# Optimization experiments

Hardware: AMD Instinct MI355X
Metric: run time of the kernel (lower is better)

The kernel has to match this reference:

```python
import jax, jax.numpy as jnp
import numpy as np

# config matching init_kwargs: stox_params=[4,2,1,1,64,2], in=64, out=128, k=3, pad=1
A_BITS = 4          # a_slices = a_bits / a_bits_per_stream = 4
W_SLICES = 2        # w_bits / w_bits_per_slice = 2
NUM_CHUNKS = 9      # ceil(64*9/64)
SUB = 64            # crossbar chunk width
ITERS = 2           # stochastic iterations
EPS = 1e-5          # BatchNorm1d eps


def ste(y, x):
    # straight-through estimator: forward y, backward identity of x
    return x + jax.lax.stop_gradient(y - x)


def unfold3x3(x):
    # torch F.unfold(x, 3, dilation=1, padding=1, stride=1): [B,C,H,W] -> [B, C*9, H*W]
    B, C, H, W = x.shape
    xp = jnp.pad(x, ((0, 0), (0, 0), (1, 1), (1, 1)))
    cols = [xp[:, :, i:i + H, j:j + W] for i in range(3) for j in range(3)]
    return jnp.stack(cols, axis=2).reshape(B, C * 9, H * W)  # (c, kh, kw) ordering


def setup_inputs() -> dict:
    key = jax.random.key(0)
    k1, k2 = jax.random.split(key)
    inputs = jax.random.normal(k1, (8, 64, 32, 32), jnp.float32)
    fan_in = 64 * 9  # kaiming_normal_ fan_in
    weight = jax.random.normal(k2, (128 * W_SLICES, 64, 3, 3), jnp.float32) * np.float32(np.sqrt(2.0 / fan_in))
    bn_gamma = jnp.ones((128 * W_SLICES,), jnp.float32)
    bn_beta = jnp.zeros((128 * W_SLICES,), jnp.float32)
    return {"inputs": inputs, "weight": weight, "bn_gamma": bn_gamma, "bn_beta": bn_beta}


def reference(inputs, weight, bn_gamma, bn_beta):
    O = weight.shape[0]  # out_channels * W_SLICES = 256
    # --- per-output-row weight standardization + 1-bit STE quantization (WeightQuantize) ---
    wf = weight.reshape(O, -1)                       # [O, Cin*9]
    bw = wf - wf.mean(-1, keepdims=True)
    bw = bw / bw.std(-1, ddof=1, keepdims=True)      # torch std is unbiased
    qw = ste(jnp.sign(bw), bw)                       # [O, Cin*9]
    # --- unfold + multi-bit input stream (create_input_stream): bit-planes stacked on batch dim ---
    a = unfold3x3(inputs)                            # [B, Cin*9, L]
    Bsz, C9, L = a.shape
    x = jnp.clip(a, 0.0, 1.0)
    q = jnp.round(x * (2 ** A_BITS - 1))
    bits = jnp.stack([jnp.floor(q / (2 ** i)) % 2 for i in range(A_BITS)], 0)  # [A,B,C9,L]
    qa = bits.reshape(A_BITS * Bsz, C9, L)
    # --- chunked crossbar linear + BatchNorm1d(train) + MTJ sign, summed over chunks/iterations ---
    out = jnp.zeros((A_BITS * Bsz, O, L), a.dtype)
    for c in range(NUM_CHUNKS):
        wk = qa[:, c * SUB:(c + 1) * SUB, :]         # [B', SUB, L]
        ww = qw[:, c * SUB:(c + 1) * SUB]            # [O, SUB]
        for _ in range(ITERS):
            lin = jnp.einsum('bcl,oc->bol', wk, ww)  # [B', O, L]
            mu = lin.mean((0, 2), keepdims=True)
            var = lin.var((0, 2), keepdims=True)     # biased, as torch BN training
            bn = bn_gamma[None, :, None] * (lin - mu) / jnp.sqrt(var + EPS) + bn_beta[None, :, None]
            out = out + ste(jnp.sign(bn), bn)        # MTJ stochastic comparator -> sign w/ STE
    # --- bit-weighted reconstructions ---
    wvec = (2.0 ** jnp.arange(W_SLICES, dtype=a.dtype)) / (2 ** W_SLICES - 1)
    out = jnp.einsum('s,bsol->bol', wvec, out.reshape(A_BITS * Bsz, W_SLICES, O // W_SLICES, L))
    avec = (2.0 ** jnp.arange(A_BITS, dtype=a.dtype)) / (2 ** A_BITS - 1)
    out = jnp.einsum('a,abol->bol', avec, out.reshape(A_BITS, Bsz, O // W_SLICES, L))
    # --- F.fold with (1,1) kernel == reshape to square spatial map ---
    P = int(np.sqrt(L))
    return out.reshape(Bsz, O // W_SLICES, P, P)
```

## Files before the change

### kernel.cpp

```cpp
#include <hip/hip_runtime.h>
#include <cstdint>
#include <cstddef>

static const size_t OFF_ACT  = 0;
static const size_t OFF_W    = OFF_ACT + 2359296;
static const size_t OFF_T    = OFF_W   + 18432;
static const size_t OFF_NS1  = OFF_T   + 18432;
static const size_t OFF_MUG  = OFF_NS1 + 9216;
static const size_t OFF_FLAG = OFF_MUG + 18432;
static const size_t OFF_WB   = OFF_FLAG + 1024;
static const size_t OFF_CQ   = OFF_WB + 147456;
static const size_t OFF_FF   = OFF_CQ + 9216;

typedef int v4i __attribute__((ext_vector_type(4)));

__device__ __forceinline__ int isgn(int e) {
  int t = e < -1 ? -1 : e;
  return t > 1 ? 1 : t;
}

__global__ __launch_bounds__(256) void k_prep(const float* __restrict__ x,
                                              const float* __restrict__ w,
                                              const float* __restrict__ gamma,
                                              const float* __restrict__ beta,
                                              int* __restrict__ T,
                                              uint64_t* __restrict__ act,
                                              uint64_t* __restrict__ wbits,
                                              int* __restrict__ flag,
                                              signed char* __restrict__ wbyte,
                                              int* __restrict__ flagF) {
  int bid = blockIdx.x;
  int tid = threadIdx.x;
  if (bid < 512) {
    int base = bid << 10;
    int vals[9];
#pragma unroll
    for (int k = 0; k < 9; ++k) vals[k] = 0;
#pragma unroll
    for (int i = 0; i < 4; ++i) {
      int px = tid + i * 256;
      int h = px >> 5, ww = px & 31;
      float v = x[base + px];
      v = fminf(fmaxf(v, 0.f), 1.f);
      int q = (int)rintf(v * 15.f);
      int pc = __popc((unsigned)q);
      vals[0] += pc;
      if (h == 0) vals[1] += pc;
      if (h == 31) vals[2] += pc;
      if (ww == 0) vals[3] += pc;
      if (ww == 31) vals[4] += pc;
      if (h == 0 && ww == 0) vals[5] += pc;
      if (h == 0 && ww == 31) vals[6] += pc;
      if (h == 31 && ww == 0) vals[7] += pc;
      if (h == 31 && ww == 31) vals[8] += pc;
    }
#pragma unroll
    for (int k = 0; k < 9; ++k)
      for (int off = 32; off; off >>= 1) vals[k] += __shfl_down(vals[k], off, 64);
    __shared__ int red[4][9];
    int wid = tid >> 6, lane = tid & 63;
    if (lane == 0)
#pragma unroll
      for (int k = 0; k < 9; ++k) red[wid][k] = vals[k];
    __syncthreads();
    if (tid < 9) T[bid * 9 + tid] = red[0][tid] + red[1][tid] + red[2][tid] + red[3][tid];
  } else if (bid < 1664) {
    int blk = bid - 512;
    int bc = blk >> 4;
    int c = bc % 9, b = bc / 9;
    int l0 = (blk & 15) << 6;
    int h0 = l0 >> 5;
    int chLo = (c * 64) / 9;
    __shared__ unsigned char qlds[8][4][34];
    for (int e = tid; e < 1024; e += 256) {
      int ci = e >> 7, rem = e & 127, ri = rem >> 5, wi = rem & 31;
      int hh = h0 - 1 + ri;
      int qv = 0;
      if ((unsigned)hh < 32u) {
        float v = x[((b * 64 + chLo + ci) << 10) + (hh << 5) + wi];
        v = fminf(fmaxf(v, 0.f), 1.f);
        qv = (int)rintf(v * 15.f);
      }
      qlds[ci][ri][wi + 1] = (unsigned char)qv;
      if (wi == 0) qlds[ci][ri][0] = 0;
      if (wi == 31) qlds[ci][ri][33] = 0;
    }
    __syncthreads();

    int half = tid & 3;
    int dl = tid >> 2;
    int l = l0 + dl;
    int h = l >> 5, w0 = l & 31;
    int hr = h - h0;
    int i9 = c * 64 + half * 16;
    int ch = i9 / 9;
    int k = i9 - ch * 9;
    int ki = k / 3, kj = k - ki * 3;
    int cch = ch - chLo;
    unsigned m0 = 0, m1 = 0, m2 = 0, m3 = 0;
#pragma unroll
    for (int jj = 0; jj < 16; ++jj) {
      int q = qlds[cch][hr + ki][w0 + kj];
      m0 |= (unsigned)(q & 1) << jj;
      m1 |= (unsigned)((q >> 1) & 1) << jj;
      m2 |= (unsigned)((q >> 2) & 1) << jj;
      m3 |= (unsigned)((q >> 3) & 1) << jj;
      if (++kj == 3) { kj = 0; if (++ki == 3) { ki = 0; ++cch; } }
    }
    size_t stride = 8 * 9 * 1024;
    size_t off = ((size_t)b * 9 + c) * 1024 + l;
    unsigned short* a16 = (unsigned short*)act;
    a16[(0 * stride + off) * 4 + half] = (unsigned short)m0;
    a16[(1 * stride + off) * 4 + half] = (unsigned short)m1;
    a16[(2 * stride + off) * 4 + half] = (unsigned short)m2;
    a16[(3 * stride + off) * 4 + half] = (unsigned short)m3;
  } else {
    int lane = tid & 63;
    int wid = tid >> 6;
    int o = (bid - 1664) * 4 + wid;
    const float* row = w + (size_t)o * 576;
    double s = 0.0;
#pragma unroll
    for (int i = 0; i < 9; ++i) s += (double)row[lane + i * 64];
    for (int off = 32; off; off >>= 1) s += __shfl_down(s, off, 64);
    s = __shfl(s, 0, 64);
    float mean = (float)(s / 576.0);
#pragma unroll
    for (int c = 0; c < 9; ++c) {
      float v = row[c * 64 + lane];
      int pos = (v - mean) > 0.f;
      unsigned long long m = __ballot(pos);
      if (lane == 0) wbits[o * 9 + c] = (uint64_t)m;
      wbyte[(c * 256 + o) * 64 + lane] = pos ? (signed char)1 : (signed char)-1;
    }
    if (lane == 0) {
      int f = (beta[o] == 0.f && gamma[o] > 0.f) ? 1 : 0;
      flag[o] = f;
      flagF[o] = f;
    }
  }
}

__global__ __launch_bounds__(256) void k_s1(const int* __restrict__ T,
                                            const uint64_t* __restrict__ wbits,
                                            const int* __restrict__ flag,
                                            const float* __restrict__ gamma,
                                            const uint64_t* __restrict__ act,
                                            int* __restrict__ negS1,
                                            int* __restrict__ cq,
                                            int* __restrict__ flagF,
                                            float2* __restrict__ MUG) {
  __shared__ int Tsh[576];
  __shared__ int Ush[9 * 65];
  int tid = threadIdx.x;
  for (int i = tid; i < 576; i += 256) {
    int acc = 0;
#pragma unroll
    for (int b = 0; b < 8; ++b) acc += T[b * 576 + i];
    Tsh[i] = acc;
  }
  __syncthreads();
  for (int i = tid; i < 576; i += 256) {
    int ch = i / 9;
    int k = i - ch * 9;
    int ki = k / 3, kj = k - ki * 3;
    const int* t = &Tsh[ch * 9];
    int u = t[0];
    if (ki == 0) u -= t[2]; else if (ki == 2) u -= t[1];
    if (kj == 0) u -= t[4]; else if (kj == 2) u -= t[3];
    if (ki == 0 && kj == 0) u += t[8];
    if (ki == 0 && kj == 2) u += t[7];
    if (ki == 2 && kj == 0) u += t[6];
    if (ki == 2 && kj == 2) u += t[5];
    Ush[(i >> 6) * 65 + (i & 63)] = u;
  }
  __syncthreads();
  int pair = blockIdx.x * 256 + tid;
  int o = pair / 9, c = pair - o * 9;
  uint64_t wv = wbits[pair];
  int tot = 0, pos = 0;
#pragma unroll 8
  for (int j = 0; j < 64; ++j) {
    int cnt = Ush[c * 65 + j];
    tot += cnt;
    if ((wv >> j) & 1) pos += cnt;
  }
  int s1 = 2 * pos - tot;
  negS1[c * 256 + o] = -s1;
  cq[c * 256 + o] = -(s1 >> 15);
  if ((s1 & 32767) == 0) atomicAnd(&flagF[o], 0);
  if (!flag[o]) {
    int s2 = 0;
    for (int i = 0; i < 32768; ++i) {
      uint64_t av = act[((size_t)(i >> 10) * 9 + c) * 1024 + (i & 1023)];
      int lin = 2 * __popcll(av & wv) - __popcll(av);
      s2 += lin * lin;
    }
    float mu = (float)s1 * (1.f / 32768.f);
    float ex2 = (float)s2 * (1.f / 32768.f);
    float var = ex2 - mu * mu;
    if (var < 0.f) var = 0.f;
    MUG[pair] = make_float2(mu, gamma[o] / sqrtf(var + 1e-5f));
  }
}

__global__ __launch_bounds__(256, 2) void k_out(const uint64_t* __restrict__ act,
                                                const signed char* __restrict__ wbyte,
                                                const int* __restrict__ negS1g,
                                                const int* __restrict__ cqg,
                                                const float2* __restrict__ MUG,
                                                const int* __restrict__ flag,
                                                const int* __restrict__ flagF,
                                                const float* __restrict__ beta,
                                                float* __restrict__ out) {
  __shared__ __align__(16) int cqsh[2304];
  int tid = threadIdx.x;
  int lt = blockIdx.x;
  int b = blockIdx.y;
  for (int i = tid; i < 2304; i += 256) cqsh[i] = cqg[i];
  __syncthreads();

  int lane = tid & 63;
  int w = __builtin_amdgcn_readfirstlane(tid >> 6);
  int row = lane & 15;
  int g = lane >> 4;
  int sh16 = (g & 1) * 16;

  int o0 = w * 32 + (lane & 31);
  int fb = flagF[o0] & flagF[o0 + 128];
  bool fastAll = (bool)__all(fb != 0);

  const v4i zacc = {0, 0, 0, 0};
  int l = lt * 16 + row;
  const char* actbyte = (const char*)act + ((size_t)b * 9 * 1024 + l) * 8 + (g >> 1) * 4;

  if (fastAll) {
    int P[4][4];
#pragma unroll
    for (int q = 0; q < 4; ++q)
#pragma unroll
      for (int r = 0; r < 4; ++r) P[q][r] = 0;

    for (int c = 0; c < 9; ++c) {
      v4i Af[4], Cin[4];
#pragma unroll
      for (int q = 0; q < 4; ++q) {
        int ot = 2 * w + (q & 1) + (q >> 1) * 8;
        Af[q] = *(const v4i*)(wbyte + ((size_t)(c * 256 + ot * 16 + row) * 64 + g * 16));
        Cin[q] = *(const v4i*)&cqsh[c * 256 + ot * 16 + g * 4];
      }
      unsigned dwv[4];
#pragma unroll
      for (int a = 0; a < 4; ++a)
        dwv[a] = *(const unsigned*)(actbyte + (size_t)a * 589824 + (size_t)c * 8192);

      int pc[4][4];
#pragma unroll
      for (int q = 0; q < 4; ++q)
#pragma unroll
        for (int r = 0; r < 4; ++r) pc[q][r] = 0;

#pragma unroll
      for (int ai = 0; ai < 4; ++ai) {
        int a = 3 - ai;
        unsigned bits = (dwv[a] >> sh16) & 0xFFFFu;
        v4i Bf;
#pragma unroll
        for (int d = 0; d < 4; ++d)
          Bf[d] = (int)((((bits >> (4 * d)) & 0xFu) * 0x00204081u) & 0x01010101u);
#pragma unroll
        for (int q = 0; q < 4; ++q) {
          v4i acc = __builtin_amdgcn_mfma_i32_16x16x64_i8(Af[q], Bf, Cin[q], 0, 0, 0);
#pragma unroll
          for (int r = 0; r < 4; ++r)
            pc[q][r] += pc[q][r] + (acc[r] > 0 ? 1 : 0);
        }
      }
#pragma unroll
      for (int q = 0; q < 4; ++q)
#pragma unroll
        for (int r = 0; r < 4; ++r) P[q][r] += pc[q][r];
    }
#pragma unroll
    for (int q2 = 0; q2 < 2; ++q2)
#pragma unroll
      for (int r = 0; r < 4; ++r) {
        int oo = (2 * w + q2) * 16 + g * 4 + r;
        int M = 2 * (P[q2][r] + 2 * P[q2 + 2][r]) - 405;
        out[((size_t)b * 128 + oo) * 1024 + l] = (float)M * (2.f / 45.f);
      }
  } else {
    int M[2][4] = {{0, 0, 0, 0}, {0, 0, 0, 0}};
    float F[2][4] = {{0.f, 0.f, 0.f, 0.f}, {0.f, 0.f, 0.f, 0.f}};
    int flv[4][4];
#pragma unroll
    for (int q = 0; q < 4; ++q) {
      int ot = 2 * w + (q & 1) + (q >> 1) * 8;
#pragma unroll
      for (int r = 0; r < 4; ++r) flv[q][r] = flag[ot * 16 + g * 4 + r];
    }
    for (int c = 0; c < 9; ++c) {
      v4i Af[4];
      int nS[4][4];
#pragma unroll
      for (int q = 0; q < 4; ++q) {
        int ot = 2 * w + (q & 1) + (q >> 1) * 8;
        Af[q] = *(const v4i*)(wbyte + ((size_t)(c * 256 + ot * 16 + row) * 64 + g * 16));
#pragma unroll
        for (int r = 0; r < 4; ++r) nS[q][r] = negS1g[c * 256 + ot * 16 + g * 4 + r];
      }
      unsigned dwv[4];
#pragma unroll
      for (int a = 0; a < 4; ++a)
        dwv[a] = *(const unsigned*)(actbyte + (size_t)a * 589824 + (size_t)c * 8192);
#pragma unroll
      for (int a = 0; a < 4; ++a) {
        unsigned bits = (dwv[a] >> sh16) & 0xFFFFu;
        v4i Bf;
#pragma unroll
        for (int d = 0; d < 4; ++d)
          Bf[d] = (int)((((bits >> (4 * d)) & 0xFu) * 0x00204081u) & 0x01010101u);
#pragma unroll
        for (int q = 0; q < 4; ++q) {
          v4i acc = __builtin_amdgcn_mfma_i32_16x16x64_i8(Af[q], Bf, zacc, 0, 0, 0);
          int ot = 2 * w + (q & 1) + (q >> 1) * 8;
#pragma unroll
          for (int r = 0; r < 4; ++r) {
            int lin = acc[r];
            if (flv[q][r]) {
              M[q & 1][r] += isgn((lin << 15) + nS[q][r]) << (a + (q >> 1));
            } else {
              int o = ot * 16 + g * 4 + r;
              float2 m2 = MUG[o * 9 + c];
              float bn = m2.y * ((float)lin - m2.x) + beta[o];
              float sg = (bn > 0.f) ? 1.f : ((bn < 0.f) ? -1.f : 0.f);
              F[q & 1][r] += sg * (float)(1 << (a + (q >> 1)));
            }
          }
        }
      }
    }
#pragma unroll
    for (int q2 = 0; q2 < 2; ++q2)
#pragma unroll
      for (int r = 0; r < 4; ++r) {
        int oo = (2 * w + q2) * 16 + g * 4 + r;
        out[((size_t)b * 128 + oo) * 1024 + l] =
            ((float)M[q2][r] + F[q2][r]) * (2.f / 45.f);
      }
  }
}

extern "C" void kernel_launch(void* const* d_in, const int* in_sizes, int n_in,
                              void* d_out, int out_size, void* d_ws, size_t ws_size,
                              hipStream_t stream) {
  const float* inputs = (const float*)d_in[0];
  const float* weight = (const float*)d_in[1];
  const float* gamma = (const float*)d_in[2];
  const float* beta = (const float*)d_in[3];
  float* out = (float*)d_out;

  char* ws = (char*)d_ws;
  uint64_t* act = (uint64_t*)(ws + OFF_ACT);
  uint64_t* wbits = (uint64_t*)(ws + OFF_W);
  int* T = (int*)(ws + OFF_T);
  int* negS1 = (int*)(ws + OFF_NS1);
  float2* MUG = (float2*)(ws + OFF_MUG);
  int* flag = (int*)(ws + OFF_FLAG);
  signed char* wbyte = (signed char*)(ws + OFF_WB);
  int* cq = (int*)(ws + OFF_CQ);
  int* flagF = (int*)(ws + OFF_FF);

  k_prep<<<1728, 256, 0, stream>>>(inputs, weight, gamma, beta, T, act, wbits, flag, wbyte, flagF);
  k_s1<<<9, 256, 0, stream>>>(T, wbits, flag, gamma, act, negS1, cq, flagF, MUG);
  k_out<<<dim3(64, 8), 256, 0, stream>>>(act, wbyte, negS1, cq, MUG, flag, flagF, beta, out);
}
```

Baseline: 89.15 us.

## Split activation bit-planes across two wave groups with LDS reduction in k_out

Doubles the k_out block to 512 threads. The upper four waves handle activation bit-planes 2-3 and the lower four handle planes 0-1, so each wave runs half the MFMA chain per chunk. Partial counts from the upper waves go through shared memory and are combined with a factor of four before the final store. This adds parallelism per output tile, since the grid is only 512 blocks, at the cost of an extra LDS buffer, a barrier and duplicated weight loads.

```diff
diff --git a/kernel.cpp b/kernel.cpp
--- a/kernel.cpp
+++ b/kernel.cpp
@@ -204,7 +204,7 @@
   }
 }
 
-__global__ __launch_bounds__(256, 2) void k_out(const uint64_t* __restrict__ act,
+__global__ __launch_bounds__(512, 4) void k_out(const uint64_t* __restrict__ act,
                                                 const signed char* __restrict__ wbyte,
                                                 const int* __restrict__ negS1g,
                                                 const int* __restrict__ cqg,
@@ -214,17 +214,21 @@
                                                 const float* __restrict__ beta,
                                                 float* __restrict__ out) {
   __shared__ __align__(16) int cqsh[2304];
+  __shared__ unsigned int part[4][16][65];
   int tid = threadIdx.x;
   int lt = blockIdx.x;
   int b = blockIdx.y;
-  for (int i = tid; i < 2304; i += 256) cqsh[i] = cqg[i];
+  for (int i = tid; i < 2304; i += 512) cqsh[i] = cqg[i];
   __syncthreads();
 
   int lane = tid & 63;
-  int w = __builtin_amdgcn_readfirstlane(tid >> 6);
+  int w8 = __builtin_amdgcn_readfirstlane(tid >> 6);
+  int w = w8 & 3;
+  int hi = w8 >> 2;
   int row = lane & 15;
   int g = lane >> 4;
   int sh16 = (g & 1) * 16;
+  int aBase = 2 * hi;
 
   int o0 = w * 32 + (lane & 31);
   int fb = flagF[o0] & flagF[o0 + 128];
@@ -233,6 +237,8 @@
   const v4i zacc = {0, 0, 0, 0};
   int l = lt * 16 + row;
   const char* actbyte = (const char*)act + ((size_t)b * 9 * 1024 + l) * 8 + (g >> 1) * 4;
+
+  unsigned pt[16];
 
   if (fastAll) {
     int P[4][4];
@@ -249,10 +255,12 @@
         Af[q] = *(const v4i*)(wbyte + ((size_t)(c * 256 + ot * 16 + row) * 64 + g * 16));
         Cin[q] = *(const v4i*)&cqsh[c * 256 + ot * 16 + g * 4];
       }
-      unsigned dwv[4];
-#pragma unroll
-      for (int a = 0; a < 4; ++a)
-        dwv[a] = *(const unsigned*)(actbyte + (size_t)a * 589824 + (size_t)c * 8192);
+      unsigned dwv[2];
+#pragma unroll
+      for (int ai = 0; ai < 2; ++ai)
+        dwv[ai] = *(const unsigned*)(actbyte +
+                                     (size_t)(aBase + ai) * 589824 +
+                                     (size_t)c * 8192);
 
       int pc[4][4];
 #pragma unroll
@@ -261,9 +269,9 @@
         for (int r = 0; r < 4; ++r) pc[q][r] = 0;
 
 #pragma unroll
-      for (int ai = 0; ai < 4; ++ai) {
-        int a = 3 - ai;
-        unsigned bits = (dwv[a] >> sh16) & 0xFFFFu;
+      for (int ai2 = 0; ai2 < 2; ++ai2) {
+        int ai = 1 - ai2;
+        unsigned bits = (dwv[ai] >> sh16) & 0xFFFFu;
         v4i Bf;
 #pragma unroll
         for (int d = 0; d < 4; ++d)
@@ -282,16 +290,12 @@
         for (int r = 0; r < 4; ++r) P[q][r] += pc[q][r];
     }
 #pragma unroll
-    for (int q2 = 0; q2 < 2; ++q2)
-#pragma unroll
-      for (int r = 0; r < 4; ++r) {
-        int oo = (2 * w + q2) * 16 + g * 4 + r;
-        int M = 2 * (P[q2][r] + 2 * P[q2 + 2][r]) - 405;
-        out[((size_t)b * 128 + oo) * 1024 + l] = (float)M * (2.f / 45.f);
-      }
+    for (int q = 0; q < 4; ++q)
+#pragma unroll
+      for (int r = 0; r < 4; ++r) pt[q * 4 + r] = (unsigned)P[q][r];
   } else {
-    int M[2][4] = {{0, 0, 0, 0}, {0, 0, 0, 0}};
-    float F[2][4] = {{0.f, 0.f, 0.f, 0.f}, {0.f, 0.f, 0.f, 0.f}};
+    int M2[2][4] = {{0, 0, 0, 0}, {0, 0, 0, 0}};
+    float F2[2][4] = {{0.f, 0.f, 0.f, 0.f}, {0.f, 0.f, 0.f, 0.f}};
     int flv[4][4];
 #pragma unroll
     for (int q = 0; q < 4; ++q) {
@@ -309,13 +313,15 @@
 #pragma unroll
         for (int r = 0; r < 4; ++r) nS[q][r] = negS1g[c * 256 + ot * 16 + g * 4 + r];
       }
-      unsigned dwv[4];
-#pragma unroll
-      for (int a = 0; a < 4; ++a)
-        dwv[a] = *(const unsigned*)(actbyte + (size_t)a * 589824 + (size_t)c * 8192);
-#pragma unroll
-      for (int a = 0; a < 4; ++a) {
-        unsigned bits = (dwv[a] >> sh16) & 0xFFFFu;
+      unsigned dwv[2];
+#pragma unroll
+      for (int ai = 0; ai < 2; ++ai)
+        dwv[ai] = *(const unsigned*)(actbyte +
+                                     (size_t)(aBase + ai) * 589824 +
+                                     (size_t)c * 8192);
+#pragma unroll
+      for (int ai = 0; ai < 2; ++ai) {
+        unsigned bits = (dwv[ai] >> sh16) & 0xFFFFu;
         v4i Bf;
 #pragma unroll
         for (int d = 0; d < 4; ++d)
@@ -328,13 +334,13 @@
           for (int r = 0; r < 4; ++r) {
             int lin = acc[r];
             if (flv[q][r]) {
-              M[q & 1][r] += isgn((lin << 15) + nS[q][r]) << (a + (q >> 1));
+              M2[q & 1][r] += isgn((lin << 15) + nS[q][r]) << (ai + (q >> 1));
             } else {
               int o = ot * 16 + g * 4 + r;
               float2 m2 = MUG[o * 9 + c];
               float bn = m2.y * ((float)lin - m2.x) + beta[o];
               float sg = (bn > 0.f) ? 1.f : ((bn < 0.f) ? -1.f : 0.f);
-              F[q & 1][r] += sg * (float)(1 << (a + (q >> 1)));
+              F2[q & 1][r] += sg * (float)(1 << (ai + (q >> 1)));
             }
           }
         }
@@ -344,10 +350,45 @@
     for (int q2 = 0; q2 < 2; ++q2)
 #pragma unroll
       for (int r = 0; r < 4; ++r) {
-        int oo = (2 * w + q2) * 16 + g * 4 + r;
-        out[((size_t)b * 128 + oo) * 1024 + l] =
-            ((float)M[q2][r] + F[q2][r]) * (2.f / 45.f);
-      }
+        pt[q2 * 4 + r] = (unsigned)M2[q2][r];
+        pt[8 + q2 * 4 + r] = __float_as_uint(F2[q2][r]);
+      }
+  }
+
+  if (hi) {
+#pragma unroll
+    for (int i = 0; i < 16; ++i) part[w][i][lane] = pt[i];
+  }
+  __syncthreads();
+  if (!hi) {
+    if (fastAll) {
+      int Pf[4][4];
+#pragma unroll
+      for (int q = 0; q < 4; ++q)
+#pragma unroll
+        for (int r = 0; r < 4; ++r)
+          Pf[q][r] = (int)pt[q * 4 + r] + 4 * (int)part[w][q * 4 + r][lane];
+#pragma unroll
+      for (int q2 = 0; q2 < 2; ++q2)
+#pragma unroll
+        for (int r = 0; r < 4; ++r) {
+          int oo = (2 * w + q2) * 16 + g * 4 + r;
+          int M = 2 * (Pf[q2][r] + 2 * Pf[q2 + 2][r]) - 405;
+          out[((size_t)b * 128 + oo) * 1024 + l] = (float)M * (2.f / 45.f);
+        }
+    } else {
+#pragma unroll
+      for (int q2 = 0; q2 < 2; ++q2)
+#pragma unroll
+        for (int r = 0; r < 4; ++r) {
+          int oo = (2 * w + q2) * 16 + g * 4 + r;
+          int Mf = (int)pt[q2 * 4 + r] + 4 * (int)part[w][q2 * 4 + r][lane];
+          float Ff = __uint_as_float(pt[8 + q2 * 4 + r]) +
+                     4.f * __uint_as_float(part[w][8 + q2 * 4 + r][lane]);
+          out[((size_t)b * 128 + oo) * 1024 + l] =
+              ((float)Mf + Ff) * (2.f / 45.f);
+        }
+    }
   }
 }
 
@@ -373,5 +414,5 @@
 
   k_prep<<<1728, 256, 0, stream>>>(inputs, weight, gamma, beta, T, act, wbits, flag, wbyte, flagF);
   k_s1<<<9, 256, 0, stream>>>(T, wbits, flag, gamma, act, negS1, cq, flagF, MUG);
-  k_out<<<dim3(64, 8), 256, 0, stream>>>(act, wbyte, negS1, cq, MUG, flag, flagF, beta, out);
+  k_out<<<dim3(64, 8), 512, 0, stream>>>(act, wbyte, negS1, cq, MUG, flag, flagF, beta, out);
 }
```

Result: no change. 88.11 us (-1.2%).
